# Kernel tuning notes

Hardware: AMD Instinct MI355X
Metric: run time of the kernel (lower is better)

The kernel has to match this reference:

```python
import jax, jax.numpy as jnp
import numpy as np

N_NODES = 100000
N_EDGES = 1280000
IN_CH = 64
OUT_CH = 64


def setup_inputs() -> dict:
    key = jax.random.key(0)
    k1, k2, k3, k4 = jax.random.split(key, 4)
    x = jax.random.normal(k1, (N_NODES, IN_CH), dtype=jnp.float32)
    edge_index = jax.random.randint(k2, (2, N_EDGES), 0, N_NODES, dtype=jnp.int64)
    # GraphConv params (glorot weight, zero bias)
    scale = jnp.sqrt(6.0 / (IN_CH + OUT_CH)).astype(jnp.float32)
    W = jax.random.uniform(k3, (IN_CH, OUT_CH), dtype=jnp.float32, minval=-scale, maxval=scale)
    b = jnp.zeros((OUT_CH,), dtype=jnp.float32)
    return {"x": x, "edge_index": edge_index, "W": W, "b": b}


def reference(x, edge_index, W, b):
    # DGL GraphConv, norm='both': out = D_in^{-1/2} A^T (D_out^{-1/2} x W) + b
    src, dst = edge_index[0], edge_index[1]
    ones = jnp.ones((src.shape[0],), dtype=x.dtype)
    out_deg = jax.ops.segment_sum(ones, src, num_segments=N_NODES)
    in_deg = jax.ops.segment_sum(ones, dst, num_segments=N_NODES)
    norm_src = jnp.where(out_deg > 0, jax.lax.rsqrt(jnp.maximum(out_deg, 1.0)), 0.0)
    norm_dst = jnp.where(in_deg > 0, jax.lax.rsqrt(jnp.maximum(in_deg, 1.0)), 0.0)
    # in_feats <= out_feats: transform first, then aggregate
    h = (x * norm_src[:, None]) @ W              # [N, OUT_CH]
    msg = h[src]                                 # gather  [E, OUT_CH]
    agg = jax.ops.segment_sum(msg, dst, num_segments=N_NODES)  # scatter-add [N, OUT_CH]
    return agg * norm_dst[:, None] + b
```

## Files before the change

### kernel.cpp

```cpp
#include <hip/hip_runtime.h>
#include <hip/hip_fp16.h>

#define CH 64
#define CAP 32
#define SPILLMAX 4096
#define RANGE 12500
#define SLICES 64
#define TILE 2048
#define EPT 8
#define BSH 9
#define BKT 512

__global__ __launch_bounds__(256) void histA_kernel(const int* __restrict__ src,
                                                    const int* __restrict__ dst,
                                                    unsigned short* __restrict__ partial,
                                                    int* __restrict__ tileHist,
                                                    int* __restrict__ nspill,
                                                    int E, int N, int R, int NT)
{
    __shared__ int h[RANGE];
    int tid = threadIdx.x;
    int bid = blockIdx.x;
    if (bid < NT) {
        if (bid == 0 && tid == 0) nspill[0] = 0;
        h[tid] = 0;
        __syncthreads();
        int e0 = bid * TILE + tid * EPT;
        if (e0 + EPT <= E) {
            const int4* dp = (const int4*)(dst + e0);
            int4 a = dp[0], b = dp[1];
            atomicAdd(&h[a.x >> BSH], 1); atomicAdd(&h[a.y >> BSH], 1);
            atomicAdd(&h[a.z >> BSH], 1); atomicAdd(&h[a.w >> BSH], 1);
            atomicAdd(&h[b.x >> BSH], 1); atomicAdd(&h[b.y >> BSH], 1);
            atomicAdd(&h[b.z >> BSH], 1); atomicAdd(&h[b.w >> BSH], 1);
        } else {
            for (int k = e0; k < E && k < e0 + EPT; ++k) atomicAdd(&h[dst[k] >> BSH], 1);
        }
        __syncthreads();
        tileHist[bid * 256 + tid] = h[tid];
    } else {
        int hb = bid - NT;
        int r  = hb % R;
        int sl = hb / R;
        int lo = r * RANGE;
        int hi = min(lo + RANGE, N);
        int span = hi - lo;
        for (int i = tid; i < span; i += 256) h[i] = 0;
        __syncthreads();
        int per = (E + SLICES - 1) / SLICES;
        int sb = sl * per, se = min(sb + per, E);
        for (int e = sb + tid * 4; e < se; e += 256 * 4) {
            if (e + 4 <= se) {
                int4 v = *(const int4*)(src + e);
                if (v.x >= lo && v.x < hi) atomicAdd(&h[v.x - lo], 1);
                if (v.y >= lo && v.y < hi) atomicAdd(&h[v.y - lo], 1);
                if (v.z >= lo && v.z < hi) atomicAdd(&h[v.z - lo], 1);
                if (v.w >= lo && v.w < hi) atomicAdd(&h[v.w - lo], 1);
            } else {
                for (int k = e; k < se; ++k) {
                    int sv = src[k];
                    if (sv >= lo && sv < hi) atomicAdd(&h[sv - lo], 1);
                }
            }
        }
        __syncthreads();
        unsigned short* pp = partial + (size_t)hb * RANGE;
        for (int i = tid; i < span; i += 256) pp[i] = (unsigned short)h[i];
    }
}

__global__ __launch_bounds__(256) void rpscaleB_kernel(const unsigned short* __restrict__ partial,
                                                       const float* __restrict__ x,
                                                       __half* __restrict__ xh,
                                                       int* __restrict__ tileHist,
                                                       int* __restrict__ totals,
                                                       int N, int R, int NT, int NPB)
{
    __shared__ float nsl[256];
    __shared__ int sm[256];
    int tid = threadIdx.x;
    int bid = blockIdx.x;
    if (bid < NPB) {
        int n0 = bid * 256;
        int n = n0 + tid;
        if (n < N) {
            int r = n / RANGE, off = n - r * RANGE;
            int s = 0;
            #pragma unroll 8
            for (int sl = 0; sl < SLICES; ++sl)
                s += partial[(size_t)(sl * R + r) * RANGE + off];
            nsl[tid] = (s > 0) ? rsqrtf((float)s) : 0.0f;
        } else {
            nsl[tid] = 0.0f;
        }
        __syncthreads();
        int sub = tid & 7;
        int nl0 = tid >> 3;
        for (int p = 0; p < 8; ++p) {
            int nl = p * 32 + nl0;
            int node = n0 + nl;
            if (node >= N) break;
            float ns = nsl[nl];
            const float4* xp = (const float4*)(x + (size_t)node * CH + sub * 8);
            float4 a = xp[0], b = xp[1];
            __half2 h0 = __floats2half2_rn(a.x * ns, a.y * ns);
            __half2 h1 = __floats2half2_rn(a.z * ns, a.w * ns);
            __half2 h2 = __floats2half2_rn(b.x * ns, b.y * ns);
            __half2 h3 = __floats2half2_rn(b.z * ns, b.w * ns);
            uint4 u;
            u.x = (unsigned)__half_as_ushort(h0.x) | ((unsigned)__half_as_ushort(h0.y) << 16);
            u.y = (unsigned)__half_as_ushort(h1.x) | ((unsigned)__half_as_ushort(h1.y) << 16);
            u.z = (unsigned)__half_as_ushort(h2.x) | ((unsigned)__half_as_ushort(h2.y) << 16);
            u.w = (unsigned)__half_as_ushort(h3.x) | ((unsigned)__half_as_ushort(h3.y) << 16);
            *(uint4*)(xh + (size_t)node * CH + sub * 8) = u;
        }
    } else {
        int b = bid - NPB;
        int C = (NT + 255) / 256;
        int vals[8];
        int s = 0;
        for (int k = 0; k < C; ++k) {
            int t = tid * C + k;
            vals[k] = (t < NT) ? tileHist[t * 256 + b] : 0;
            s += vals[k];
        }
        sm[tid] = s;
        __syncthreads();
        for (int d = 1; d < 256; d <<= 1) {
            int v = (tid >= d) ? sm[tid - d] : 0;
            __syncthreads();
            sm[tid] += v;
            __syncthreads();
        }
        int off = (tid > 0) ? sm[tid - 1] : 0;
        for (int k = 0; k < C; ++k) {
            int t = tid * C + k;
            if (t < NT) { tileHist[t * 256 + b] = off; off += vals[k]; }
        }
        if (tid == 255) totals[b] = sm[255];
    }
}

__global__ __launch_bounds__(256) void binC_kernel(const int* __restrict__ src,
                                                   const int* __restrict__ dst,
                                                   const int* __restrict__ tileBase,
                                                   const int* __restrict__ totals,
                                                   int* __restrict__ sorted, int E, int NB)
{
    __shared__ int sm[256];
    __shared__ int cur[256];
    int tid = threadIdx.x;
    int t = blockIdx.x;
    sm[tid] = (tid < NB) ? totals[tid] : 0;
    __syncthreads();
    for (int d = 1; d < 256; d <<= 1) {
        int v = (tid >= d) ? sm[tid - d] : 0;
        __syncthreads();
        sm[tid] += v;
        __syncthreads();
    }
    int bb = (tid > 0) ? sm[tid - 1] : 0;
    cur[tid] = (tid < NB) ? bb + tileBase[t * 256 + tid] : 0;
    __syncthreads();
    int e0 = t * TILE + tid * EPT;
    int s[EPT], d[EPT];
    int nk = 0;
    if (e0 + EPT <= E) {
        const int4* sp = (const int4*)(src + e0);
        const int4* dp = (const int4*)(dst + e0);
        int4 a = sp[0], b = sp[1], c = dp[0], f = dp[1];
        s[0]=a.x; s[1]=a.y; s[2]=a.z; s[3]=a.w; s[4]=b.x; s[5]=b.y; s[6]=b.z; s[7]=b.w;
        d[0]=c.x; d[1]=c.y; d[2]=c.z; d[3]=c.w; d[4]=f.x; d[5]=f.y; d[6]=f.z; d[7]=f.w;
        nk = EPT;
    } else {
        for (int k = 0; e0 + k < E && k < EPT; ++k) { s[k] = src[e0+k]; d[k] = dst[e0+k]; nk++; }
    }
    for (int k = 0; k < nk; ++k) {
        int p = d[k] >> BSH;
        int pos = atomicAdd(&cur[p], 1);
        sorted[pos] = (s[k] << BSH) | (d[k] & (BKT - 1));
    }
}

__global__ __launch_bounds__(256) void binD_kernel(const int* __restrict__ sorted,
                                                   const int* __restrict__ totals,
                                                   int* __restrict__ bucket,
                                                   int* __restrict__ cnt,
                                                   int* __restrict__ spill,
                                                   int* __restrict__ nspill, int N, int NB)
{
    __shared__ int sm[256];
    __shared__ int lc[BKT];
    int b = blockIdx.x, tid = threadIdx.x;
    sm[tid] = (tid < NB) ? totals[tid] : 0;
    lc[tid] = 0; lc[tid + 256] = 0;
    __syncthreads();
    for (int d = 1; d < 256; d <<= 1) {
        int v = (tid >= d) ? sm[tid - d] : 0;
        __syncthreads();
        sm[tid] += v;
        __syncthreads();
    }
    int beg = (b > 0) ? sm[b - 1] : 0;
    int end = sm[b];
    int nbase = b << BSH;
    for (int i = beg + tid; i < end; i += 256) {
        int v = sorted[i];
        int sv = v >> BSH;
        int dl = v & (BKT - 1);
        int pos = atomicAdd(&lc[dl], 1);
        if (pos < CAP) {
            bucket[(size_t)(nbase + dl) * CAP + pos] = sv;
        } else {
            int sp = atomicAdd(nspill, 1);
            if (sp < SPILLMAX) { spill[2*sp] = nbase + dl; spill[2*sp+1] = sv; }
        }
    }
    __syncthreads();
    int n0 = nbase + tid;
    if (n0 < N) cnt[n0] = lc[tid];
    int n1 = nbase + 256 + tid;
    if (n1 < N) cnt[n1] = lc[256 + tid];
}

__global__ __launch_bounds__(256) void agg_kernel(const __half* __restrict__ xh,
                                                  const int* __restrict__ bucket,
                                                  const int* __restrict__ cnt,
                                                  const int* __restrict__ spill,
                                                  const int* __restrict__ nspill,
                                                  __half* __restrict__ aggh, int N)
{
    int node = (blockIdx.x * blockDim.x + threadIdx.x) >> 5;
    int sl = threadIdx.x & 31;
    if (node >= N) return;
    int c = cnt[node];
    int m = (c < CAP) ? c : CAP;
    const int* bp = bucket + (size_t)node * CAP;
    float ax0 = 0, ay0 = 0, ax1 = 0, ay1 = 0, ax2 = 0, ay2 = 0, ax3 = 0, ay3 = 0;
    int j = 0;
    for (; j + 8 <= m; j += 8) {
        int4 va = *(const int4*)(bp + j);
        int4 vb = *(const int4*)(bp + j + 4);
        float2 f0 = __half22float2(*(const __half2*)(xh + (size_t)va.x * CH + sl * 2));
        float2 f1 = __half22float2(*(const __half2*)(xh + (size_t)va.y * CH + sl * 2));
        float2 f2 = __half22float2(*(const __half2*)(xh + (size_t)va.z * CH + sl * 2));
        float2 f3 = __half22float2(*(const __half2*)(xh + (size_t)va.w * CH + sl * 2));
        float2 f4 = __half22float2(*(const __half2*)(xh + (size_t)vb.x * CH + sl * 2));
        float2 f5 = __half22float2(*(const __half2*)(xh + (size_t)vb.y * CH + sl * 2));
        float2 f6 = __half22float2(*(const __half2*)(xh + (size_t)vb.z * CH + sl * 2));
        float2 f7 = __half22float2(*(const __half2*)(xh + (size_t)vb.w * CH + sl * 2));
        ax0 += f0.x + f4.x; ay0 += f0.y + f4.y;
        ax1 += f1.x + f5.x; ay1 += f1.y + f5.y;
        ax2 += f2.x + f6.x; ay2 += f2.y + f6.y;
        ax3 += f3.x + f7.x; ay3 += f3.y + f7.y;
    }
    for (; j + 4 <= m; j += 4) {
        int4 va = *(const int4*)(bp + j);
        float2 f0 = __half22float2(*(const __half2*)(xh + (size_t)va.x * CH + sl * 2));
        float2 f1 = __half22float2(*(const __half2*)(xh + (size_t)va.y * CH + sl * 2));
        float2 f2 = __half22float2(*(const __half2*)(xh + (size_t)va.z * CH + sl * 2));
        float2 f3 = __half22float2(*(const __half2*)(xh + (size_t)va.w * CH + sl * 2));
        ax0 += f0.x; ay0 += f0.y;
        ax1 += f1.x; ay1 += f1.y;
        ax2 += f2.x; ay2 += f2.y;
        ax3 += f3.x; ay3 += f3.y;
    }
    for (; j < m; ++j) {
        float2 f = __half22float2(*(const __half2*)(xh + (size_t)bp[j] * CH + sl * 2));
        ax0 += f.x; ay0 += f.y;
    }
    if (c > CAP) {
        int ns = *nspill;
        if (ns > SPILLMAX) ns = SPILLMAX;
        for (int i = 0; i < ns; ++i) {
            if (spill[2 * i] == node) {
                float2 f = __half22float2(*(const __half2*)(xh + (size_t)spill[2 * i + 1] * CH + sl * 2));
                ax0 += f.x; ay0 += f.y;
            }
        }
    }
    float nd = (c > 0) ? rsqrtf((float)c) : 0.0f;
    float rx = ((ax0 + ax1) + (ax2 + ax3)) * nd;
    float ry = ((ay0 + ay1) + (ay2 + ay3)) * nd;
    *(__half2*)(aggh + (size_t)node * CH + sl * 2) = __floats2half2_rn(rx, ry);
}

__global__ __launch_bounds__(256) void gemm_out_kernel(const __half* __restrict__ aggh,
                                                       const float* __restrict__ W,
                                                       const float* __restrict__ bias,
                                                       float* __restrict__ out, int N)
{
    int g = blockIdx.x * 256 + threadIdx.x;
    int waveId = __builtin_amdgcn_readfirstlane(g >> 6);
    int lane = threadIdx.x & 63;
    int quarter = waveId & 3;
    int row = ((waveId >> 2) << 6) + lane;
    if (row >= N) return;
    const int cbase = quarter * 16;
    float acc[16];
    #pragma unroll
    for (int i = 0; i < 16; ++i) acc[i] = 0.0f;
    const __half* xp = aggh + (size_t)row * CH;
    for (int k0 = 0; k0 < CH; k0 += 8) {
        uint4 u = *(const uint4*)(xp + k0);
        const __half2* hp = (const __half2*)&u;
        float xk[8];
        #pragma unroll
        for (int j = 0; j < 4; ++j) {
            float2 f = __half22float2(hp[j]);
            xk[2 * j] = f.x; xk[2 * j + 1] = f.y;
        }
        #pragma unroll
        for (int kk = 0; kk < 8; ++kk) {
            const float* wrow = W + (k0 + kk) * CH + cbase;
            #pragma unroll
            for (int q = 0; q < 4; ++q) {
                float4 w = *(const float4*)(wrow + q * 4);
                acc[q * 4 + 0] += xk[kk] * w.x;
                acc[q * 4 + 1] += xk[kk] * w.y;
                acc[q * 4 + 2] += xk[kk] * w.z;
                acc[q * 4 + 3] += xk[kk] * w.w;
            }
        }
    }
    float* op = out + (size_t)row * CH + cbase;
    #pragma unroll
    for (int q = 0; q < 4; ++q) {
        float4 b = *(const float4*)(bias + cbase + q * 4);
        float4 o;
        o.x = acc[q * 4 + 0] + b.x;
        o.y = acc[q * 4 + 1] + b.y;
        o.z = acc[q * 4 + 2] + b.z;
        o.w = acc[q * 4 + 3] + b.w;
        *(float4*)(op + q * 4) = o;
    }
}

extern "C" void kernel_launch(void* const* d_in, const int* in_sizes, int n_in,
                              void* d_out, int out_size, void* d_ws, size_t ws_size,
                              hipStream_t stream)
{
    const float* x    = (const float*)d_in[0];
    const int*   edge = (const int*)d_in[1];
    const float* W    = (const float*)d_in[2];
    const float* bias = (const float*)d_in[3];
    float* out = (float*)d_out;

    int N = in_sizes[0] / CH;
    int E = in_sizes[1] / 2;
    const int* src = edge;
    const int* dst = edge + E;
    int R   = (N + RANGE - 1) / RANGE;
    int NT  = (E + TILE - 1) / TILE;
    int NB  = (N + BKT - 1) >> BSH;
    int NPB = (N + 255) / 256;

    int* nspill  = (int*)d_ws;
    int* spill   = nspill + 64;
    int* cnt     = spill + 2 * SPILLMAX;
    int* bucket  = cnt + N;
    unsigned short* partial = (unsigned short*)(bucket + (size_t)N * CAP);
    int* tileHist = (int*)(partial + (size_t)SLICES * R * RANGE);
    int* totals   = tileHist + NT * 256;
    int* sorted   = (int*)partial;
    size_t endoff = (char*)(totals + 320) - (char*)d_ws;
    size_t xoff = (endoff + 255) & ~(size_t)255;
    __half* xh = (__half*)((char*)d_ws + xoff);
    size_t aoff = ((xoff + (size_t)N * CH * sizeof(__half)) + 255) & ~(size_t)255;
    __half* aggh = (__half*)((char*)d_ws + aoff);

    histA_kernel<<<NT + R * SLICES, 256, 0, stream>>>(src, dst, partial, tileHist,
                                                      nspill, E, N, R, NT);
    rpscaleB_kernel<<<NPB + NB, 256, 0, stream>>>(partial, x, xh, tileHist, totals,
                                                  N, R, NT, NPB);
    binC_kernel<<<NT, 256, 0, stream>>>(src, dst, tileHist, totals, sorted, E, NB);
    binD_kernel<<<NB, 256, 0, stream>>>(sorted, totals, bucket, cnt, spill, nspill, N, NB);
    agg_kernel<<<((size_t)N * 32 + 255) / 256, 256, 0, stream>>>(xh, bucket, cnt, spill,
                                                                 nspill, aggh, N);
    int nwaves = 4 * ((N + 63) / 64);
    gemm_out_kernel<<<(nwaves + 3) / 4, 256, 0, stream>>>(aggh, W, bias, out, N);
}
```

Measured before the change: 109.7 us.

## Stage binned edges in LDS for coalesced writes; grid-stride aggregation kernel

The binning kernel now ranks each edge within its tile by bucket using LDS atomics, prefix-scans the local counts, and stages the packed edges in shared memory in bucket order. It then writes them out contiguously per bucket, with a binary search to find each slot's bucket. This replaces scattered per-edge global stores with mostly contiguous runs. Separately, the aggregation kernel becomes a grid-stride loop over a fixed 4096-block grid instead of one half-wave per node. The extra LDS, scans and barriers add overhead per tile.

```diff
diff --git a/kernel.cpp b/kernel.cpp
--- a/kernel.cpp
+++ b/kernel.cpp
@@ -148,10 +148,14 @@
                                                    int* __restrict__ sorted, int E, int NB)
 {
     __shared__ int sm[256];
-    __shared__ int cur[256];
+    __shared__ int gb[256];
+    __shared__ int lcnt[256];
+    __shared__ int lbase[256];
+    __shared__ int slotVal[TILE];
     int tid = threadIdx.x;
     int t = blockIdx.x;
     sm[tid] = (tid < NB) ? totals[tid] : 0;
+    lcnt[tid] = 0;
     __syncthreads();
     for (int d = 1; d < 256; d <<= 1) {
         int v = (tid >= d) ? sm[tid - d] : 0;
@@ -160,10 +164,10 @@
         __syncthreads();
     }
     int bb = (tid > 0) ? sm[tid - 1] : 0;
-    cur[tid] = (tid < NB) ? bb + tileBase[t * 256 + tid] : 0;
+    gb[tid] = (tid < NB) ? bb + tileBase[t * 256 + tid] : 0;
     __syncthreads();
     int e0 = t * TILE + tid * EPT;
-    int s[EPT], d[EPT];
+    int s[EPT], d[EPT], rk[EPT], pb[EPT];
     int nk = 0;
     if (e0 + EPT <= E) {
         const int4* sp = (const int4*)(src + e0);
@@ -176,9 +180,32 @@
         for (int k = 0; e0 + k < E && k < EPT; ++k) { s[k] = src[e0+k]; d[k] = dst[e0+k]; nk++; }
     }
     for (int k = 0; k < nk; ++k) {
-        int p = d[k] >> BSH;
-        int pos = atomicAdd(&cur[p], 1);
-        sorted[pos] = (s[k] << BSH) | (d[k] & (BKT - 1));
+        pb[k] = d[k] >> BSH;
+        rk[k] = atomicAdd(&lcnt[pb[k]], 1);
+    }
+    __syncthreads();
+    sm[tid] = lcnt[tid];
+    __syncthreads();
+    for (int dd = 1; dd < 256; dd <<= 1) {
+        int v = (tid >= dd) ? sm[tid - dd] : 0;
+        __syncthreads();
+        sm[tid] += v;
+        __syncthreads();
+    }
+    lbase[tid] = (tid > 0) ? sm[tid - 1] : 0;
+    int total = sm[255];
+    __syncthreads();
+    for (int k = 0; k < nk; ++k)
+        slotVal[lbase[pb[k]] + rk[k]] = (s[k] << BSH) | (d[k] & (BKT - 1));
+    __syncthreads();
+    for (int i = tid; i < total; i += 256) {
+        int lo = 0, hi = 255;
+        #pragma unroll
+        for (int st = 0; st < 8; ++st) {
+            int mid = (lo + hi + 1) >> 1;
+            if (lbase[mid] <= i) lo = mid; else hi = mid - 1;
+        }
+        sorted[gb[lo] + (i - lbase[lo])] = slotVal[i];
     }
 }
 
@@ -230,59 +257,61 @@
                                                   const int* __restrict__ nspill,
                                                   __half* __restrict__ aggh, int N)
 {
-    int node = (blockIdx.x * blockDim.x + threadIdx.x) >> 5;
+    int hw0 = (blockIdx.x * blockDim.x + threadIdx.x) >> 5;
+    int nHW = (gridDim.x * blockDim.x) >> 5;
     int sl = threadIdx.x & 31;
-    if (node >= N) return;
-    int c = cnt[node];
-    int m = (c < CAP) ? c : CAP;
-    const int* bp = bucket + (size_t)node * CAP;
-    float ax0 = 0, ay0 = 0, ax1 = 0, ay1 = 0, ax2 = 0, ay2 = 0, ax3 = 0, ay3 = 0;
-    int j = 0;
-    for (; j + 8 <= m; j += 8) {
-        int4 va = *(const int4*)(bp + j);
-        int4 vb = *(const int4*)(bp + j + 4);
-        float2 f0 = __half22float2(*(const __half2*)(xh + (size_t)va.x * CH + sl * 2));
-        float2 f1 = __half22float2(*(const __half2*)(xh + (size_t)va.y * CH + sl * 2));
-        float2 f2 = __half22float2(*(const __half2*)(xh + (size_t)va.z * CH + sl * 2));
-        float2 f3 = __half22float2(*(const __half2*)(xh + (size_t)va.w * CH + sl * 2));
-        float2 f4 = __half22float2(*(const __half2*)(xh + (size_t)vb.x * CH + sl * 2));
-        float2 f5 = __half22float2(*(const __half2*)(xh + (size_t)vb.y * CH + sl * 2));
-        float2 f6 = __half22float2(*(const __half2*)(xh + (size_t)vb.z * CH + sl * 2));
-        float2 f7 = __half22float2(*(const __half2*)(xh + (size_t)vb.w * CH + sl * 2));
-        ax0 += f0.x + f4.x; ay0 += f0.y + f4.y;
-        ax1 += f1.x + f5.x; ay1 += f1.y + f5.y;
-        ax2 += f2.x + f6.x; ay2 += f2.y + f6.y;
-        ax3 += f3.x + f7.x; ay3 += f3.y + f7.y;
-    }
-    for (; j + 4 <= m; j += 4) {
-        int4 va = *(const int4*)(bp + j);
-        float2 f0 = __half22float2(*(const __half2*)(xh + (size_t)va.x * CH + sl * 2));
-        float2 f1 = __half22float2(*(const __half2*)(xh + (size_t)va.y * CH + sl * 2));
-        float2 f2 = __half22float2(*(const __half2*)(xh + (size_t)va.z * CH + sl * 2));
-        float2 f3 = __half22float2(*(const __half2*)(xh + (size_t)va.w * CH + sl * 2));
-        ax0 += f0.x; ay0 += f0.y;
-        ax1 += f1.x; ay1 += f1.y;
-        ax2 += f2.x; ay2 += f2.y;
-        ax3 += f3.x; ay3 += f3.y;
-    }
-    for (; j < m; ++j) {
-        float2 f = __half22float2(*(const __half2*)(xh + (size_t)bp[j] * CH + sl * 2));
-        ax0 += f.x; ay0 += f.y;
-    }
-    if (c > CAP) {
-        int ns = *nspill;
-        if (ns > SPILLMAX) ns = SPILLMAX;
-        for (int i = 0; i < ns; ++i) {
-            if (spill[2 * i] == node) {
-                float2 f = __half22float2(*(const __half2*)(xh + (size_t)spill[2 * i + 1] * CH + sl * 2));
-                ax0 += f.x; ay0 += f.y;
+    for (int node = hw0; node < N; node += nHW) {
+        int c = cnt[node];
+        int m = (c < CAP) ? c : CAP;
+        const int* bp = bucket + (size_t)node * CAP;
+        float ax0 = 0, ay0 = 0, ax1 = 0, ay1 = 0, ax2 = 0, ay2 = 0, ax3 = 0, ay3 = 0;
+        int j = 0;
+        for (; j + 8 <= m; j += 8) {
+            int4 va = *(const int4*)(bp + j);
+            int4 vb = *(const int4*)(bp + j + 4);
+            float2 f0 = __half22float2(*(const __half2*)(xh + (size_t)va.x * CH + sl * 2));
+            float2 f1 = __half22float2(*(const __half2*)(xh + (size_t)va.y * CH + sl * 2));
+            float2 f2 = __half22float2(*(const __half2*)(xh + (size_t)va.z * CH + sl * 2));
+            float2 f3 = __half22float2(*(const __half2*)(xh + (size_t)va.w * CH + sl * 2));
+            float2 f4 = __half22float2(*(const __half2*)(xh + (size_t)vb.x * CH + sl * 2));
+            float2 f5 = __half22float2(*(const __half2*)(xh + (size_t)vb.y * CH + sl * 2));
+            float2 f6 = __half22float2(*(const __half2*)(xh + (size_t)vb.z * CH + sl * 2));
+            float2 f7 = __half22float2(*(const __half2*)(xh + (size_t)vb.w * CH + sl * 2));
+            ax0 += f0.x + f4.x; ay0 += f0.y + f4.y;
+            ax1 += f1.x + f5.x; ay1 += f1.y + f5.y;
+            ax2 += f2.x + f6.x; ay2 += f2.y + f6.y;
+            ax3 += f3.x + f7.x; ay3 += f3.y + f7.y;
+        }
+        for (; j + 4 <= m; j += 4) {
+            int4 va = *(const int4*)(bp + j);
+            float2 f0 = __half22float2(*(const __half2*)(xh + (size_t)va.x * CH + sl * 2));
+            float2 f1 = __half22float2(*(const __half2*)(xh + (size_t)va.y * CH + sl * 2));
+            float2 f2 = __half22float2(*(const __half2*)(xh + (size_t)va.z * CH + sl * 2));
+            float2 f3 = __half22float2(*(const __half2*)(xh + (size_t)va.w * CH + sl * 2));
+            ax0 += f0.x; ay0 += f0.y;
+            ax1 += f1.x; ay1 += f1.y;
+            ax2 += f2.x; ay2 += f2.y;
+            ax3 += f3.x; ay3 += f3.y;
+        }
+        for (; j < m; ++j) {
+            float2 f = __half22float2(*(const __half2*)(xh + (size_t)bp[j] * CH + sl * 2));
+            ax0 += f.x; ay0 += f.y;
+        }
+        if (c > CAP) {
+            int ns = *nspill;
+            if (ns > SPILLMAX) ns = SPILLMAX;
+            for (int i = 0; i < ns; ++i) {
+                if (spill[2 * i] == node) {
+                    float2 f = __half22float2(*(const __half2*)(xh + (size_t)spill[2 * i + 1] * CH + sl * 2));
+                    ax0 += f.x; ay0 += f.y;
+                }
             }
         }
-    }
-    float nd = (c > 0) ? rsqrtf((float)c) : 0.0f;
-    float rx = ((ax0 + ax1) + (ax2 + ax3)) * nd;
-    float ry = ((ay0 + ay1) + (ay2 + ay3)) * nd;
-    *(__half2*)(aggh + (size_t)node * CH + sl * 2) = __floats2half2_rn(rx, ry);
+        float nd = (c > 0) ? rsqrtf((float)c) : 0.0f;
+        float rx = ((ax0 + ax1) + (ax2 + ax3)) * nd;
+        float ry = ((ay0 + ay1) + (ay2 + ay3)) * nd;
+        *(__half2*)(aggh + (size_t)node * CH + sl * 2) = __floats2half2_rn(rx, ry);
+    }
 }
 
 __global__ __launch_bounds__(256) void gemm_out_kernel(const __half* __restrict__ aggh,
@@ -375,8 +404,7 @@
                                                   N, R, NT, NPB);
     binC_kernel<<<NT, 256, 0, stream>>>(src, dst, tileHist, totals, sorted, E, NB);
     binD_kernel<<<NB, 256, 0, stream>>>(sorted, totals, bucket, cnt, spill, nspill, N, NB);
-    agg_kernel<<<((size_t)N * 32 + 255) / 256, 256, 0, stream>>>(xh, bucket, cnt, spill,
-                                                                 nspill, aggh, N);
+    agg_kernel<<<4096, 256, 0, stream>>>(xh, bucket, cnt, spill, nspill, aggh, N);
     int nwaves = 4 * ((N + 63) / 64);
     gemm_out_kernel<<<(nwaves + 3) / 4, 256, 0, stream>>>(aggh, W, bias, out, N);
 }
```

Measured after the change: 109.0 us. About the same (-0.7%).
